# Optimization experiments

Hardware: AMD Instinct MI355X
Metric: run time of the kernel (lower is better)

Reference implementation:

```python
import jax, jax.numpy as jnp
import numpy as np

N = 100000          # nodes
E = 3200000         # edges (before self-loops)
IN = 128            # gcn_in_size
DIMS = [128, 256, 256]  # ndim_out
HID = 200           # mlp_hid_size
CLS = 2             # n_classes
BN_EPS = 1e-5


def setup_inputs() -> dict:
    key = jax.random.key(0)
    ks = jax.random.split(key, 12)
    inp = {}
    inp["features"] = jax.random.normal(ks[0], (N, IN), jnp.float32)
    inp["src"] = jax.random.randint(ks[1], (E,), 0, N)
    inp["dst"] = jax.random.randint(ks[2], (E,), 0, N)
    dims = [IN] + DIMS
    i = 3
    for l in range(3):
        inp[f"W{l}"] = jax.random.normal(ks[i], (dims[l], dims[l + 1]), jnp.float32) / np.sqrt(dims[l]).astype(np.float32)
        inp[f"b{l}"] = jnp.zeros((dims[l + 1],), jnp.float32)
        i += 1
    inp["Wm1"] = jax.random.normal(ks[i], (DIMS[-1], HID), jnp.float32) / np.sqrt(DIMS[-1]).astype(np.float32); i += 1
    inp["bm1"] = jnp.zeros((HID,), jnp.float32)
    inp["gamma"] = jnp.ones((HID,), jnp.float32)
    inp["beta"] = jnp.zeros((HID,), jnp.float32)
    inp["Wm2"] = jax.random.normal(ks[i], (HID, CLS), jnp.float32) / np.sqrt(HID).astype(np.float32)
    inp["bm2"] = jnp.zeros((CLS,), jnp.float32)
    return inp


def reference(features, src, dst, W0, b0, W1, b1, W2, b2, Wm1, bm1, gamma, beta, Wm2, bm2):
    # dgl.add_self_loop
    nodes = jnp.arange(N, dtype=src.dtype)
    s = jnp.concatenate([src, nodes])
    d = jnp.concatenate([dst, nodes])
    ones = jnp.ones(s.shape[0], jnp.float32)
    # DGL GraphConv norm='both': D_out^{-1/2} on src side, D_in^{-1/2} on dst side
    deg_out = jax.ops.segment_sum(ones, s, num_segments=N)  # >=1 due to self-loops
    deg_in = jax.ops.segment_sum(ones, d, num_segments=N)
    norm_src = jax.lax.rsqrt(deg_out)[:, None]
    norm_dst = jax.lax.rsqrt(deg_in)[:, None]

    h = features
    for W, b in ((W0, b0), (W1, b1), (W2, b2)):
        msg = (h * norm_src)[s]                                  # [E+N, din] gather
        agg = jax.ops.segment_sum(msg, d, num_segments=N) * norm_dst
        h = jax.nn.relu(agg @ W + b)                             # GraphConv activation=relu
        # gcn dropout: identity in eval mode

    # MLPPredictor: Dropout(eval=id) -> Linear -> ReLU -> BatchNorm1d (batch stats) -> Linear
    z = jax.nn.relu(h @ Wm1 + bm1)
    mu = z.mean(axis=0)
    var = z.var(axis=0)
    z = (z - mu) * jax.lax.rsqrt(var + BN_EPS) * gamma + beta
    return z @ Wm2 + bm2
```

## Files before the change

kernel.cpp:

```cpp
#include <hip/hip_runtime.h>

#define NN 100000
#define NE 3200000
#define NBUK 196
#define CAP 18432
#define NAB 512
#define ECHK ((NE + NAB - 1)/NAB)

typedef unsigned short u16;
typedef unsigned int u32;
typedef __attribute__((ext_vector_type(8))) short short8v;
typedef __attribute__((ext_vector_type(4))) float f32x4;

__device__ __forceinline__ u16 f2b(float f){
  u32 u = __float_as_uint(f);
  u32 r = (u + 0x7fffu + ((u >> 16) & 1u)) >> 16;
  return (u16)r;
}
__device__ __forceinline__ float b2f(u16 b){
  return __uint_as_float(((u32)b) << 16);
}

__global__ void k_misc(const float* __restrict__ W0, const float* __restrict__ W1,
                       const float* __restrict__ W2, const float* __restrict__ Wm1,
                       u16* __restrict__ wt0, u16* __restrict__ wt1,
                       u16* __restrict__ wt2, u16* __restrict__ wtm1,
                       u32* __restrict__ gcntD, u32* __restrict__ gcntS,
                       float* __restrict__ bns, float* __restrict__ bnq){
  int i = blockIdx.x*256 + threadIdx.x;
  if(i < 16384){
    int n = i >> 7, k = i & 127;
    wt0[i] = f2b(W0[k*128 + n]);
  } else if((i -= 16384) < 32768){
    int n = i >> 7, k = i & 127;
    wt1[i] = f2b(W1[k*256 + n]);
  } else if((i -= 32768) < 65536){
    int n = i >> 8, k = i & 255;
    wt2[i] = f2b(W2[k*256 + n]);
  } else if((i -= 65536) < 51200){
    int n = i >> 8, k = i & 255;
    wtm1[i] = f2b(Wm1[k*200 + n]);
  } else if((i -= 51200) < 512){
    if(i < 256) gcntD[i] = 0; else gcntS[i-256] = 0;
  } else if((i -= 512) < 400){
    if(i < 200) bns[i] = 0.f; else bnq[i-200] = 0.f;
  }
}

__global__ __launch_bounds__(256) void k_bin(const int* __restrict__ src,
                      const int* __restrict__ dst,
                      u32* __restrict__ gcntD, u32* __restrict__ gcntS,
                      u32* __restrict__ pairD, u16* __restrict__ keyS){
  __shared__ u32 cntD[NBUK], cntS[NBUK], offD[NBUK], offS[NBUK];
  int t = threadIdx.x, b = blockIdx.x;
  for(int j=t; j<NBUK; j+=256){ cntD[j]=0; cntS[j]=0; }
  __syncthreads();
  int start = b*ECHK, end = min(start + ECHK, NE);
  for(int e = start + t; e < end; e += 256){
    atomicAdd(&cntD[dst[e] >> 9], 1u);
    atomicAdd(&cntS[src[e] >> 9], 1u);
  }
  __syncthreads();
  for(int j=t; j<NBUK; j+=256){
    offD[j] = atomicAdd(&gcntD[j], cntD[j]);
    offS[j] = atomicAdd(&gcntS[j], cntS[j]);
    cntD[j] = 0; cntS[j] = 0;
  }
  __syncthreads();
  for(int e = start + t; e < end; e += 256){
    int d = dst[e], s = src[e];
    int bd = d >> 9, bs = s >> 9;
    u32 pd = offD[bd] + atomicAdd(&cntD[bd], 1u);
    u32 ps = offS[bs] + atomicAdd(&cntS[bs], 1u);
    if(pd < CAP) pairD[bd*CAP + pd] = ((u32)s << 9) | (u32)(d & 511);
    if(ps < CAP) keyS[bs*CAP + ps] = (u16)(s & 511);
  }
}

__global__ void k_boff(const u32* __restrict__ gcntD, u32* __restrict__ bOffD){
  if(threadIdx.x==0){
    u32 run = 0;
    for(int i=0;i<NBUK;i++){ bOffD[i]=run; run+=gcntD[i]; }
  }
}

__global__ __launch_bounds__(256) void k_bucket_dst(
    const u32* __restrict__ pairD, const u32* __restrict__ gcntD,
    const u32* __restrict__ bOffD, int* __restrict__ degi,
    float* __restrict__ nd, int* __restrict__ rowp, int* __restrict__ csr){
  __shared__ u32 hist[512], excl[512], fill[512], tsum[256];
  int t = threadIdx.x, b = blockIdx.x;
  int base = b << 9;
  hist[t] = 0; hist[t+256] = 0; fill[t] = 0; fill[t+256] = 0;
  __syncthreads();
  int nD = gcntD[b];
  const u32* pp = pairD + (size_t)b*CAP;
  for(int i=t; i<nD; i+=256) atomicAdd(&hist[pp[i] & 511], 1u);
  __syncthreads();
  u32 a0 = hist[2*t], a1 = hist[2*t+1];
  tsum[t] = a0 + a1;
  __syncthreads();
  for(int off=1; off<256; off<<=1){
    u32 v = (t>=off) ? tsum[t-off] : 0;
    __syncthreads();
    tsum[t] += v;
    __syncthreads();
  }
  u32 texc = tsum[t] - (a0 + a1);
  excl[2*t] = texc; excl[2*t+1] = texc + a0;
  __syncthreads();
  u32 bo = bOffD[b];
  #pragma unroll
  for(int j=0;j<2;j++){
    int local = t + j*256;
    int v = base + local;
    if(v < NN){
      int cnt = (int)hist[local];
      degi[v] = cnt + 1;
      nd[v] = rsqrtf((float)(cnt + 1));
      rowp[v] = (int)(bo + excl[local]);
    }
  }
  __syncthreads();
  for(int i=t; i<nD; i+=256){
    u32 w = pp[i];
    int local = w & 511;
    u32 pos = bo + excl[local] + atomicAdd(&fill[local], 1u);
    csr[pos] = (int)(w >> 9);
  }
}

__global__ __launch_bounds__(256) void k_bucket_src(
    const u16* __restrict__ keyS, const u32* __restrict__ gcntS,
    float* __restrict__ ns){
  __shared__ u32 hist[512];
  int t = threadIdx.x, b = blockIdx.x;
  hist[t] = 0; hist[t+256] = 0;
  __syncthreads();
  int nS = gcntS[b];
  const u16* kp = keyS + (size_t)b*CAP;
  for(int i=t; i<nS; i+=256) atomicAdd(&hist[kp[i]], 1u);
  __syncthreads();
  #pragma unroll
  for(int j=0;j<2;j++){
    int local = t + j*256;
    int v = (b << 9) + local;
    if(v < NN) ns[v] = rsqrtf((float)(hist[local] + 1));
  }
}

__global__ void k_cvt(const float* __restrict__ f, const float* __restrict__ ns,
                      u16* __restrict__ out){
  int i = blockIdx.x*256 + threadIdx.x;
  if(i >= NN*32) return;
  int row = i >> 5;
  float nsv = ns[row];
  float4 v = *(const float4*)(f + (size_t)i*4);
  u32 w0 = (u32)f2b(v.x*nsv) | ((u32)f2b(v.y*nsv) << 16);
  u32 w1 = (u32)f2b(v.z*nsv) | ((u32)f2b(v.w*nsv) << 16);
  *(uint2*)(out + (size_t)i*4) = make_uint2(w0, w1);
}

template<int DIM>
__global__ void k_spmm8(const u16* __restrict__ h, const int* __restrict__ rowp,
                        const int* __restrict__ degi, const int* __restrict__ csr,
                        const float* __restrict__ nd, u16* __restrict__ out){
  constexpr int EP = 8, G = 8;
  constexpr int NV = DIM/(G*8);
  int w = (blockIdx.x*blockDim.x + threadIdx.x) >> 6;
  int lane = threadIdx.x & 63;
  if(w >= NN) return;
  int g = lane >> 3, gl = lane & 7;
  const uint4* hv = (const uint4*)h;
  float acc[NV*8];
  #pragma unroll
  for(int i=0;i<NV*8;i++) acc[i]=0.f;

  int start = rowp[w];
  int vcnt = degi[w];

  uint4 cur[NV];
  int k = g;
  if(k < vcnt){
    int n0 = (k == 0) ? w : csr[start + k - 1];
    #pragma unroll
    for(int v4=0; v4<NV; v4++) cur[v4] = hv[(size_t)n0*(DIM/8) + gl*NV + v4];

    int kn = k + EP;
    int nn = (kn < vcnt) ? csr[start + kn - 1] : 0;

    while(true){
      bool more = (kn < vcnt);
      uint4 nxt[NV];
      if(more){
        #pragma unroll
        for(int v4=0; v4<NV; v4++) nxt[v4] = hv[(size_t)nn*(DIM/8) + gl*NV + v4];
      }
      int k2 = kn + EP;
      if(k2 < vcnt) nn = csr[start + k2 - 1];
      #pragma unroll
      for(int v4=0; v4<NV; v4++){
        u32 wd[4] = {cur[v4].x, cur[v4].y, cur[v4].z, cur[v4].w};
        #pragma unroll
        for(int i=0;i<4;i++){
          acc[v4*8 + 2*i]   += __uint_as_float(wd[i] << 16);
          acc[v4*8 + 2*i+1] += __uint_as_float(wd[i] & 0xffff0000u);
        }
      }
      if(!more) break;
      #pragma unroll
      for(int v4=0; v4<NV; v4++) cur[v4] = nxt[v4];
      kn = k2;
    }
  }

  #pragma unroll
  for(int i=0;i<NV*8;i++){
    acc[i] += __shfl_xor(acc[i], 8);
    acc[i] += __shfl_xor(acc[i], 16);
    acc[i] += __shfl_xor(acc[i], 32);
  }
  if(g == 0){
    float ndv = nd[w];
    #pragma unroll
    for(int v4=0; v4<NV; v4++){
      u32 o[4];
      #pragma unroll
      for(int i=0;i<4;i++){
        o[i] = (u32)f2b(acc[v4*8+2*i]*ndv) | ((u32)f2b(acc[v4*8+2*i+1]*ndv) << 16);
      }
      *(uint4*)(out + (size_t)w*DIM + (gl*NV + v4)*8) = make_uint4(o[0],o[1],o[2],o[3]);
    }
  }
}

template<int OUTMODE>
__global__ __launch_bounds__(256) void k_gemm_mfma(
    const u16* __restrict__ A, const u16* __restrict__ Bt,
    const float* __restrict__ bias, const float* __restrict__ ns,
    u16* __restrict__ outb, float* __restrict__ outf,
    float* __restrict__ bns, float* __restrict__ bnq,
    int M, int K, int Nn)
{
  __shared__ u16 As[128*32];
  __shared__ u16 Bs[128*32];
  int t = threadIdx.x;
  int wave = t >> 6, lane = t & 63;
  int l15 = lane & 15, l4 = lane >> 4;
  int wr = (wave >> 1)*64, wc = (wave & 1)*64;
  int row0 = blockIdx.y*128, col0 = blockIdx.x*128;

  f32x4 acc[4][4];
  #pragma unroll
  for(int m=0;m<4;m++)
    #pragma unroll
    for(int n=0;n<4;n++) acc[m][n] = (f32x4)(0.f);

  int st_r = t >> 1;
  int kc0 = (t & 1)*2;
  int sw  = (st_r >> 1) & 3;
  int c0 = kc0 ^ sw, c1 = (kc0+1) ^ sw;
  bool avalid = (row0 + st_r) < M;
  bool bvalid = (col0 + st_r) < Nn;
  const u16* Ap = A  + (size_t)(row0 + st_r)*K + kc0*8;
  const u16* Bp = Bt + (size_t)(col0 + st_r)*K + kc0*8;

  for(int k0 = 0; k0 < K; k0 += 32){
    uint4 va0 = make_uint4(0,0,0,0), va1 = va0, vb0 = va0, vb1 = va0;
    if(avalid){ va0 = *(const uint4*)(Ap + k0); va1 = *(const uint4*)(Ap + k0 + 8); }
    if(bvalid){ vb0 = *(const uint4*)(Bp + k0); vb1 = *(const uint4*)(Bp + k0 + 8); }
    __syncthreads();
    *(uint4*)&As[st_r*32 + c0*8] = va0;
    *(uint4*)&As[st_r*32 + c1*8] = va1;
    *(uint4*)&Bs[st_r*32 + c0*8] = vb0;
    *(uint4*)&Bs[st_r*32 + c1*8] = vb1;
    __syncthreads();

    short8v af[4], bg[4];
    #pragma unroll
    for(int m=0;m<4;m++){
      int r = wr + m*16 + l15;
      int kc = l4 ^ ((r >> 1) & 3);
      af[m] = *(const short8v*)&As[r*32 + kc*8];
    }
    #pragma unroll
    for(int n=0;n<4;n++){
      int r = wc + n*16 + l15;
      int kc = l4 ^ ((r >> 1) & 3);
      bg[n] = *(const short8v*)&Bs[r*32 + kc*8];
    }
    #pragma unroll
    for(int m=0;m<4;m++)
      #pragma unroll
      for(int n=0;n<4;n++)
        acc[m][n] = __builtin_amdgcn_mfma_f32_16x16x32_bf16(af[m], bg[n], acc[m][n], 0, 0, 0);
    __syncthreads();
  }

  float nsv[4][4];
  if(OUTMODE == 0){
    #pragma unroll
    for(int m=0;m<4;m++)
      #pragma unroll
      for(int r=0;r<4;r++){
        int gr = row0 + wr + m*16 + l4*4 + r;
        nsv[m][r] = (gr < M) ? ns[gr] : 0.f;
      }
  }
  #pragma unroll
  for(int n=0;n<4;n++){
    int gc = col0 + wc + n*16 + l15;
    float bv = (gc < Nn) ? bias[gc] : 0.f;
    float s = 0.f, q = 0.f;
    #pragma unroll
    for(int m=0;m<4;m++){
      #pragma unroll
      for(int r=0;r<4;r++){
        int gr = row0 + wr + m*16 + l4*4 + r;
        bool ok = (gr < M) && (gc < Nn);
        float v = ok ? fmaxf(acc[m][n][r] + bv, 0.f) : 0.f;
        if(ok){
          if(OUTMODE == 0)      outb[(size_t)gr*Nn + gc] = f2b(v * nsv[m][r]);
          else if(OUTMODE == 1) outb[(size_t)gr*Nn + gc] = f2b(v);
          else                  outf[(size_t)gr*Nn + gc] = v;
        }
        if(OUTMODE == 2){ s += v; q += v*v; }
      }
    }
    if(OUTMODE == 2){
      s += __shfl_xor(s, 16); s += __shfl_xor(s, 32);
      q += __shfl_xor(q, 16); q += __shfl_xor(q, 32);
      if(l4 == 0 && gc < Nn){ atomicAdd(&bns[gc], s); atomicAdd(&bnq[gc], q); }
    }
  }
}

__global__ void k_bn2(const float* __restrict__ bns, const float* __restrict__ bnq,
                      const float* __restrict__ gamma, const float* __restrict__ beta,
                      const float* __restrict__ Wm2, const float* __restrict__ bm2,
                      float* __restrict__ w2a, float* __restrict__ cc2){
  __shared__ float c0s[200];
  int t = threadIdx.x;
  if(t<200){
    float mu  = bns[t] * (1.0f/NN);
    float var = bnq[t] * (1.0f/NN) - mu*mu;
    float a   = rsqrtf(var + 1e-5f) * gamma[t];
    w2a[t*2+0] = a*Wm2[t*2+0];
    w2a[t*2+1] = a*Wm2[t*2+1];
    c0s[t] = beta[t] - mu*a;
  }
  __syncthreads();
  if(t<2){
    float cst = bm2[t];
    for(int k=0;k<200;k++) cst += c0s[k]*Wm2[k*2+t];
    cc2[t] = cst;
  }
}

__global__ void k_final(const float* __restrict__ z, const float* __restrict__ w2a,
                        const float* __restrict__ cc2, float* __restrict__ out){
  int lane = threadIdx.x & 63;
  int gw = (blockIdx.x*blockDim.x + threadIdx.x) >> 6;
  if(gw >= NN) return;
  const float* zr = z + (size_t)gw*200;
  float p0=0.f, p1=0.f;
  #pragma unroll
  for(int i=0;i<4;i++){
    int c = lane + i*64;
    if(c<200){ float x=zr[c]; p0 += x*w2a[c*2+0]; p1 += x*w2a[c*2+1]; }
  }
  for(int off=32; off>0; off>>=1){
    p0 += __shfl_down(p0, off);
    p1 += __shfl_down(p1, off);
  }
  if(lane==0){ out[gw*2+0] = p0 + cc2[0]; out[gw*2+1] = p1 + cc2[1]; }
}

extern "C" void kernel_launch(void* const* d_in, const int* in_sizes, int n_in,
                              void* d_out, int out_size, void* d_ws, size_t ws_size,
                              hipStream_t stream) {
  const float* features = (const float*)d_in[0];
  const int*   src = (const int*)d_in[1];
  const int*   dst = (const int*)d_in[2];
  const float* W0  = (const float*)d_in[3];
  const float* b0  = (const float*)d_in[4];
  const float* W1  = (const float*)d_in[5];
  const float* b1  = (const float*)d_in[6];
  const float* W2  = (const float*)d_in[7];
  const float* b2  = (const float*)d_in[8];
  const float* Wm1 = (const float*)d_in[9];
  const float* bm1 = (const float*)d_in[10];
  const float* gamma = (const float*)d_in[11];
  const float* beta  = (const float*)d_in[12];
  const float* Wm2 = (const float*)d_in[13];
  const float* bm2 = (const float*)d_in[14];
  float* out = (float*)d_out;

  char* p = (char*)d_ws;
  auto alloc = [&](size_t bytes)->void*{
    void* r = (void*)p; p += (bytes + 255) & ~(size_t)255; return r;
  };
  u16*   X    = (u16*)alloc((size_t)NN*256*2);
  u16*   Y    = (u16*)alloc((size_t)NN*256*2);
  float* z    = (float*)alloc((size_t)NN*200*4);
  int*   csr  = (int*)alloc((size_t)NE*4);
  int*   rowp = (int*)alloc((size_t)NN*4);
  int*   degi = (int*)alloc((size_t)NN*4);
  float* ns   = (float*)alloc((size_t)NN*4);
  float* nd   = (float*)alloc((size_t)NN*4);
  u32*   gcntD = (u32*)alloc(256*4);
  u32*   gcntS = (u32*)alloc(256*4);
  u32*   bOffD = (u32*)alloc(256*4);
  float* bns  = (float*)alloc(200*4);
  float* bnq  = (float*)alloc(200*4);
  float* w2a  = (float*)alloc(400*4);
  float* cc2  = (float*)alloc(2*4);
  u16*   wt0  = (u16*)alloc((size_t)128*128*2);
  u16*   wt1  = (u16*)alloc((size_t)256*128*2);
  u16*   wt2  = (u16*)alloc((size_t)256*256*2);
  u16*   wtm1 = (u16*)alloc((size_t)200*256*2);
  u32*   pairD = (u32*)z;
  u16*   keyS  = (u16*)((char*)z + (size_t)32*1024*1024);

  k_misc<<<(16384+32768+65536+51200+512+400 + 255)/256, 256, 0, stream>>>(
      W0, W1, W2, Wm1, wt0, wt1, wt2, wtm1, gcntD, gcntS, bns, bnq);
  k_bin<<<NAB, 256, 0, stream>>>(src, dst, gcntD, gcntS, pairD, keyS);
  k_boff<<<1, 64, 0, stream>>>(gcntD, bOffD);
  k_bucket_dst<<<NBUK, 256, 0, stream>>>(pairD, gcntD, bOffD, degi, nd, rowp, csr);
  k_bucket_src<<<NBUK, 256, 0, stream>>>(keyS, gcntS, ns);

  k_cvt<<<(NN*32 + 255)/256, 256, 0, stream>>>(features, ns, X);

  int sblk = (NN + 3)/4;
  int gblk = (NN + 127)/128;

  k_spmm8<128><<<sblk, 256, 0, stream>>>(X, rowp, degi, csr, nd, Y);
  k_gemm_mfma<0><<<dim3(1,gblk), 256, 0, stream>>>(Y, wt0, b0, ns, X, nullptr, nullptr, nullptr, NN, 128, 128);
  k_spmm8<128><<<sblk, 256, 0, stream>>>(X, rowp, degi, csr, nd, Y);
  k_gemm_mfma<0><<<dim3(2,gblk), 256, 0, stream>>>(Y, wt1, b1, ns, X, nullptr, nullptr, nullptr, NN, 128, 256);
  k_spmm8<256><<<sblk, 256, 0, stream>>>(X, rowp, degi, csr, nd, Y);
  k_gemm_mfma<1><<<dim3(2,gblk), 256, 0, stream>>>(Y, wt2, b2, nullptr, X, nullptr, nullptr, nullptr, NN, 256, 256);
  k_gemm_mfma<2><<<dim3(2,gblk), 256, 0, stream>>>(X, wtm1, bm1, nullptr, nullptr, z, bns, bnq, NN, 256, 200);

  k_bn2<<<1, 256, 0, stream>>>(bns, bnq, gamma, beta, Wm2, bm2, w2a, cc2);
  k_final<<<sblk, 256, 0, stream>>>(z, w2a, cc2, out);
}
```

Measured before the change: 806.5 us.

## Restructure GEMM to stage whole weight tile in LDS and read A directly

The MFMA GEMM now loads the entire weight tile (128 columns × full K) into swizzled LDS once per block, and reads A fragments straight from global memory into registers. This removes the per-K-step LDS staging of A and the repeated barriers. K is now a template parameter so the loop fully unrolls, and the wtm1 allocation is enlarged so out-of-range weight rows are padded. The A reads are no longer row-guarded, so the last partial row block reads past M and relies on the buffer being large enough. The LDS footprint grows with K, which could lower occupancy.

```diff
diff --git a/kernel.cpp b/kernel.cpp
--- a/kernel.cpp
+++ b/kernel.cpp
@@ -234,67 +234,68 @@
   }
 }
 
-template<int OUTMODE>
-__global__ __launch_bounds__(256) void k_gemm_mfma(
+template<int OUTMODE, int KK>
+__global__ __launch_bounds__(256) void k_gemm2(
     const u16* __restrict__ A, const u16* __restrict__ Bt,
     const float* __restrict__ bias, const float* __restrict__ ns,
     u16* __restrict__ outb, float* __restrict__ outf,
     float* __restrict__ bns, float* __restrict__ bnq,
-    int M, int K, int Nn)
+    int M, int Nn)
 {
-  __shared__ u16 As[128*32];
-  __shared__ u16 Bs[128*32];
+  constexpr int NCH = KK/8;
+  __shared__ u16 Bs[128*KK];
   int t = threadIdx.x;
   int wave = t >> 6, lane = t & 63;
   int l15 = lane & 15, l4 = lane >> 4;
   int wr = (wave >> 1)*64, wc = (wave & 1)*64;
   int row0 = blockIdx.y*128, col0 = blockIdx.x*128;
 
+  {
+    int r = t >> 1;
+    int cbase = (t & 1)*(NCH/2);
+    int sw = r & 7;
+    bool valid = (col0 + r) < Nn;
+    const uint4* gp = (const uint4*)(Bt + (size_t)(col0 + r)*KK);
+    uint4* lp = (uint4*)&Bs[r*KK];
+    #pragma unroll
+    for(int j=0;j<NCH/2;j++){
+      int c = cbase + j;
+      uint4 v = valid ? gp[c] : make_uint4(0,0,0,0);
+      lp[c ^ sw] = v;
+    }
+  }
+  __syncthreads();
+
   f32x4 acc[4][4];
   #pragma unroll
   for(int m=0;m<4;m++)
     #pragma unroll
     for(int n=0;n<4;n++) acc[m][n] = (f32x4)(0.f);
 
-  int st_r = t >> 1;
-  int kc0 = (t & 1)*2;
-  int sw  = (st_r >> 1) & 3;
-  int c0 = kc0 ^ sw, c1 = (kc0+1) ^ sw;
-  bool avalid = (row0 + st_r) < M;
-  bool bvalid = (col0 + st_r) < Nn;
-  const u16* Ap = A  + (size_t)(row0 + st_r)*K + kc0*8;
-  const u16* Bp = Bt + (size_t)(col0 + st_r)*K + kc0*8;
-
-  for(int k0 = 0; k0 < K; k0 += 32){
-    uint4 va0 = make_uint4(0,0,0,0), va1 = va0, vb0 = va0, vb1 = va0;
-    if(avalid){ va0 = *(const uint4*)(Ap + k0); va1 = *(const uint4*)(Ap + k0 + 8); }
-    if(bvalid){ vb0 = *(const uint4*)(Bp + k0); vb1 = *(const uint4*)(Bp + k0 + 8); }
-    __syncthreads();
-    *(uint4*)&As[st_r*32 + c0*8] = va0;
-    *(uint4*)&As[st_r*32 + c1*8] = va1;
-    *(uint4*)&Bs[st_r*32 + c0*8] = vb0;
-    *(uint4*)&Bs[st_r*32 + c1*8] = vb1;
-    __syncthreads();
-
-    short8v af[4], bg[4];
+  #pragma unroll
+  for(int k0=0; k0<KK; k0+=64){
+    short8v af[4][2], bg[4][2];
     #pragma unroll
     for(int m=0;m<4;m++){
-      int r = wr + m*16 + l15;
-      int kc = l4 ^ ((r >> 1) & 3);
-      af[m] = *(const short8v*)&As[r*32 + kc*8];
+      const u16* ap = A + (size_t)(row0 + wr + m*16 + l15)*KK + k0 + l4*8;
+      af[m][0] = *(const short8v*)ap;
+      af[m][1] = *(const short8v*)(ap + 32);
     }
     #pragma unroll
     for(int n=0;n<4;n++){
       int r = wc + n*16 + l15;
-      int kc = l4 ^ ((r >> 1) & 3);
-      bg[n] = *(const short8v*)&Bs[r*32 + kc*8];
-    }
-    #pragma unroll
-    for(int m=0;m<4;m++)
-      #pragma unroll
-      for(int n=0;n<4;n++)
-        acc[m][n] = __builtin_amdgcn_mfma_f32_16x16x32_bf16(af[m], bg[n], acc[m][n], 0, 0, 0);
-    __syncthreads();
+      int sw = r & 7;
+      int base = r*NCH + (k0>>3);
+      bg[n][0] = *(const short8v*)&Bs[(base + ((l4    ) ^ sw))*8];
+      bg[n][1] = *(const short8v*)&Bs[(base + ((l4 + 4) ^ sw))*8];
+    }
+    #pragma unroll
+    for(int ks=0; ks<2; ks++)
+      #pragma unroll
+      for(int m=0;m<4;m++)
+        #pragma unroll
+        for(int n=0;n<4;n++)
+          acc[m][n] = __builtin_amdgcn_mfma_f32_16x16x32_bf16(af[m][ks], bg[n][ks], acc[m][n], 0, 0, 0);
   }
 
   float nsv[4][4];
@@ -418,7 +419,7 @@
   u16*   wt0  = (u16*)alloc((size_t)128*128*2);
   u16*   wt1  = (u16*)alloc((size_t)256*128*2);
   u16*   wt2  = (u16*)alloc((size_t)256*256*2);
-  u16*   wtm1 = (u16*)alloc((size_t)200*256*2);
+  u16*   wtm1 = (u16*)alloc((size_t)256*256*2);
   u32*   pairD = (u32*)z;
   u16*   keyS  = (u16*)((char*)z + (size_t)32*1024*1024);
 
@@ -435,12 +436,12 @@
   int gblk = (NN + 127)/128;
 
   k_spmm8<128><<<sblk, 256, 0, stream>>>(X, rowp, degi, csr, nd, Y);
-  k_gemm_mfma<0><<<dim3(1,gblk), 256, 0, stream>>>(Y, wt0, b0, ns, X, nullptr, nullptr, nullptr, NN, 128, 128);
+  k_gemm2<0,128><<<dim3(1,gblk), 256, 0, stream>>>(Y, wt0, b0, ns, X, nullptr, nullptr, nullptr, NN, 128);
   k_spmm8<128><<<sblk, 256, 0, stream>>>(X, rowp, degi, csr, nd, Y);
-  k_gemm_mfma<0><<<dim3(2,gblk), 256, 0, stream>>>(Y, wt1, b1, ns, X, nullptr, nullptr, nullptr, NN, 128, 256);
+  k_gemm2<0,128><<<dim3(2,gblk), 256, 0, stream>>>(Y, wt1, b1, ns, X, nullptr, nullptr, nullptr, NN, 256);
   k_spmm8<256><<<sblk, 256, 0, stream>>>(X, rowp, degi, csr, nd, Y);
-  k_gemm_mfma<1><<<dim3(2,gblk), 256, 0, stream>>>(Y, wt2, b2, nullptr, X, nullptr, nullptr, nullptr, NN, 256, 256);
-  k_gemm_mfma<2><<<dim3(2,gblk), 256, 0, stream>>>(X, wtm1, bm1, nullptr, nullptr, z, bns, bnq, NN, 256, 200);
+  k_gemm2<1,256><<<dim3(2,gblk), 256, 0, stream>>>(Y, wt2, b2, nullptr, X, nullptr, nullptr, nullptr, NN, 256);
+  k_gemm2<2,256><<<dim3(2,gblk), 256, 0, stream>>>(X, wtm1, bm1, nullptr, nullptr, z, bns, bnq, NN, 200);
 
   k_bn2<<<1, 256, 0, stream>>>(bns, bnq, gamma, beta, Wm2, bm2, w2a, cc2);
   k_final<<<sblk, 256, 0, stream>>>(z, w2a, cc2, out);
```

Result: slower. 852.5 us (+5.7%).

## Widen GEMM tiles to cover full output width and store MLP activations as bf16

Applied to the files above, without the earlier changes.

The MFMA GEMM now uses 512-thread blocks with a 128x256 tile, so each block covers the whole output width. Each row tile of A is loaded once instead of once per column block. K is a compile-time template parameter so the k-loop fully unrolls, and the trailing barrier inside the loop is dropped. The hidden MLP activation z is written and read back as bf16 instead of fp32, halving that traffic at some precision cost in the final projection.

```diff
diff --git a/kernel.cpp b/kernel.cpp
--- a/kernel.cpp
+++ b/kernel.cpp
@@ -234,21 +234,21 @@
   }
 }
 
-template<int OUTMODE>
-__global__ __launch_bounds__(256) void k_gemm_mfma(
+template<int OUTMODE, int KK>
+__global__ __launch_bounds__(512) void k_gemm8(
     const u16* __restrict__ A, const u16* __restrict__ Bt,
     const float* __restrict__ bias, const float* __restrict__ ns,
-    u16* __restrict__ outb, float* __restrict__ outf,
+    u16* __restrict__ outb,
     float* __restrict__ bns, float* __restrict__ bnq,
-    int M, int K, int Nn)
+    int M, int Nn)
 {
   __shared__ u16 As[128*32];
-  __shared__ u16 Bs[128*32];
+  __shared__ u16 Bs[256*32];
   int t = threadIdx.x;
   int wave = t >> 6, lane = t & 63;
   int l15 = lane & 15, l4 = lane >> 4;
-  int wr = (wave >> 1)*64, wc = (wave & 1)*64;
-  int row0 = blockIdx.y*128, col0 = blockIdx.x*128;
+  int wr = (wave >> 2)*64, wc = (wave & 3)*64;
+  int row0 = blockIdx.y*128;
 
   f32x4 acc[4][4];
   #pragma unroll
@@ -256,24 +256,24 @@
     #pragma unroll
     for(int n=0;n<4;n++) acc[m][n] = (f32x4)(0.f);
 
-  int st_r = t >> 1;
-  int kc0 = (t & 1)*2;
-  int sw  = (st_r >> 1) & 3;
-  int c0 = kc0 ^ sw, c1 = (kc0+1) ^ sw;
-  bool avalid = (row0 + st_r) < M;
-  bool bvalid = (col0 + st_r) < Nn;
-  const u16* Ap = A  + (size_t)(row0 + st_r)*K + kc0*8;
-  const u16* Bp = Bt + (size_t)(col0 + st_r)*K + kc0*8;
-
-  for(int k0 = 0; k0 < K; k0 += 32){
-    uint4 va0 = make_uint4(0,0,0,0), va1 = va0, vb0 = va0, vb1 = va0;
-    if(avalid){ va0 = *(const uint4*)(Ap + k0); va1 = *(const uint4*)(Ap + k0 + 8); }
+  int ar = t >> 2, ac = t & 3;
+  int swA = (ar >> 1) & 3;
+  int br = t >> 1, bc0 = (t & 1)*2;
+  int swB = (br >> 1) & 3;
+  bool avalid = (row0 + ar) < M;
+  bool bvalid = br < Nn;
+  const u16* Ap = A  + (size_t)(row0 + ar)*KK + ac*8;
+  const u16* Bp = Bt + (size_t)br*KK + bc0*8;
+
+  #pragma unroll
+  for(int k0 = 0; k0 < KK; k0 += 32){
+    uint4 va = make_uint4(0,0,0,0), vb0 = va, vb1 = va;
+    if(avalid) va = *(const uint4*)(Ap + k0);
     if(bvalid){ vb0 = *(const uint4*)(Bp + k0); vb1 = *(const uint4*)(Bp + k0 + 8); }
     __syncthreads();
-    *(uint4*)&As[st_r*32 + c0*8] = va0;
-    *(uint4*)&As[st_r*32 + c1*8] = va1;
-    *(uint4*)&Bs[st_r*32 + c0*8] = vb0;
-    *(uint4*)&Bs[st_r*32 + c1*8] = vb1;
+    *(uint4*)&As[ar*32 + (ac ^ swA)*8] = va;
+    *(uint4*)&Bs[br*32 + (bc0 ^ swB)*8] = vb0;
+    *(uint4*)&Bs[br*32 + ((bc0+1) ^ swB)*8] = vb1;
     __syncthreads();
 
     short8v af[4], bg[4];
@@ -294,7 +294,6 @@
       #pragma unroll
       for(int n=0;n<4;n++)
         acc[m][n] = __builtin_amdgcn_mfma_f32_16x16x32_bf16(af[m], bg[n], acc[m][n], 0, 0, 0);
-    __syncthreads();
   }
 
   float nsv[4][4];
@@ -309,7 +308,7 @@
   }
   #pragma unroll
   for(int n=0;n<4;n++){
-    int gc = col0 + wc + n*16 + l15;
+    int gc = wc + n*16 + l15;
     float bv = (gc < Nn) ? bias[gc] : 0.f;
     float s = 0.f, q = 0.f;
     #pragma unroll
@@ -320,9 +319,8 @@
         bool ok = (gr < M) && (gc < Nn);
         float v = ok ? fmaxf(acc[m][n][r] + bv, 0.f) : 0.f;
         if(ok){
-          if(OUTMODE == 0)      outb[(size_t)gr*Nn + gc] = f2b(v * nsv[m][r]);
-          else if(OUTMODE == 1) outb[(size_t)gr*Nn + gc] = f2b(v);
-          else                  outf[(size_t)gr*Nn + gc] = v;
+          if(OUTMODE == 0) outb[(size_t)gr*Nn + gc] = f2b(v * nsv[m][r]);
+          else             outb[(size_t)gr*Nn + gc] = f2b(v);
         }
         if(OUTMODE == 2){ s += v; q += v*v; }
       }
@@ -357,17 +355,24 @@
   }
 }
 
-__global__ void k_final(const float* __restrict__ z, const float* __restrict__ w2a,
+__global__ void k_final(const u16* __restrict__ z, const float* __restrict__ w2a,
                         const float* __restrict__ cc2, float* __restrict__ out){
   int lane = threadIdx.x & 63;
   int gw = (blockIdx.x*blockDim.x + threadIdx.x) >> 6;
   if(gw >= NN) return;
-  const float* zr = z + (size_t)gw*200;
+  const u32* zr = (const u32*)(z + (size_t)gw*200);
   float p0=0.f, p1=0.f;
   #pragma unroll
-  for(int i=0;i<4;i++){
-    int c = lane + i*64;
-    if(c<200){ float x=zr[c]; p0 += x*w2a[c*2+0]; p1 += x*w2a[c*2+1]; }
+  for(int i=0;i<2;i++){
+    int wd = lane + i*64;
+    if(wd < 100){
+      u32 v = zr[wd];
+      float x0 = __uint_as_float(v << 16);
+      float x1 = __uint_as_float(v & 0xffff0000u);
+      int e = wd*2;
+      p0 += x0*w2a[e*2+0] + x1*w2a[e*2+2];
+      p1 += x0*w2a[e*2+1] + x1*w2a[e*2+3];
+    }
   }
   for(int off=32; off>0; off>>=1){
     p0 += __shfl_down(p0, off);
@@ -402,7 +407,7 @@
   };
   u16*   X    = (u16*)alloc((size_t)NN*256*2);
   u16*   Y    = (u16*)alloc((size_t)NN*256*2);
-  float* z    = (float*)alloc((size_t)NN*200*4);
+  u16*   zb   = (u16*)alloc((size_t)NN*200*2);
   int*   csr  = (int*)alloc((size_t)NE*4);
   int*   rowp = (int*)alloc((size_t)NN*4);
   int*   degi = (int*)alloc((size_t)NN*4);
@@ -418,9 +423,9 @@
   u16*   wt0  = (u16*)alloc((size_t)128*128*2);
   u16*   wt1  = (u16*)alloc((size_t)256*128*2);
   u16*   wt2  = (u16*)alloc((size_t)256*256*2);
-  u16*   wtm1 = (u16*)alloc((size_t)200*256*2);
-  u32*   pairD = (u32*)z;
-  u16*   keyS  = (u16*)((char*)z + (size_t)32*1024*1024);
+  u16*   wtm1 = (u16*)alloc((size_t)256*256*2);
+  u32*   pairD = (u32*)zb;
+  u16*   keyS  = (u16*)((char*)zb + (size_t)15*1024*1024);
 
   k_misc<<<(16384+32768+65536+51200+512+400 + 255)/256, 256, 0, stream>>>(
       W0, W1, W2, Wm1, wt0, wt1, wt2, wtm1, gcntD, gcntS, bns, bnq);
@@ -435,13 +440,13 @@
   int gblk = (NN + 127)/128;
 
   k_spmm8<128><<<sblk, 256, 0, stream>>>(X, rowp, degi, csr, nd, Y);
-  k_gemm_mfma<0><<<dim3(1,gblk), 256, 0, stream>>>(Y, wt0, b0, ns, X, nullptr, nullptr, nullptr, NN, 128, 128);
+  k_gemm8<0,128><<<dim3(1,gblk), 512, 0, stream>>>(Y, wt0, b0, ns, X, nullptr, nullptr, NN, 128);
   k_spmm8<128><<<sblk, 256, 0, stream>>>(X, rowp, degi, csr, nd, Y);
-  k_gemm_mfma<0><<<dim3(2,gblk), 256, 0, stream>>>(Y, wt1, b1, ns, X, nullptr, nullptr, nullptr, NN, 128, 256);
+  k_gemm8<0,128><<<dim3(1,gblk), 512, 0, stream>>>(Y, wt1, b1, ns, X, nullptr, nullptr, NN, 256);
   k_spmm8<256><<<sblk, 256, 0, stream>>>(X, rowp, degi, csr, nd, Y);
-  k_gemm_mfma<1><<<dim3(2,gblk), 256, 0, stream>>>(Y, wt2, b2, nullptr, X, nullptr, nullptr, nullptr, NN, 256, 256);
-  k_gemm_mfma<2><<<dim3(2,gblk), 256, 0, stream>>>(X, wtm1, bm1, nullptr, nullptr, z, bns, bnq, NN, 256, 200);
+  k_gemm8<1,256><<<dim3(1,gblk), 512, 0, stream>>>(Y, wt2, b2, nullptr, X, nullptr, nullptr, NN, 256);
+  k_gemm8<2,256><<<dim3(1,gblk), 512, 0, stream>>>(X, wtm1, bm1, nullptr, zb, bns, bnq, NN, 200);
 
   k_bn2<<<1, 256, 0, stream>>>(bns, bnq, gamma, beta, Wm2, bm2, w2a, cc2);
-  k_final<<<sblk, 256, 0, stream>>>(z, w2a, cc2, out);
-}
+  k_final<<<sblk, 256, 0, stream>>>(zb, w2a, cc2, out);
+}
```

Result: faster. 766.5 us (-5.0%).
